# Performance work log

Measured on AMD Instinct MI355X. Metric: run time of the kernel, lower is better.

The kernel has to match this reference:

```python
import jax, jax.numpy as jnp
import numpy as np

N = 8192  # number of candidates being ranked


def setup_inputs() -> dict:
    key = jax.random.key(0)
    k1, k2 = jax.random.split(key)
    logits = jax.random.normal(k1, (N,), dtype=jnp.float32)
    rankings = jax.random.randint(k2, (N,), 0, N).astype(jnp.int64)
    return {"logits": logits, "rankings": rankings}


def reference(logits, rankings):
    # Vectorized WeightedRankNetLoss:
    #   loss = (1/N) * sum_{i<j, r_i<r_j} log(1 + exp(logits[j]-logits[i])) / (r_i + r_j)
    n = logits.shape[0]
    idx = jnp.arange(n)
    # pair selected iff i < j AND rankings[i] < rankings[j]
    pair_mask = (idx[:, None] < idx[None, :]) & (rankings[:, None] < rankings[None, :])
    r = rankings.astype(logits.dtype)
    rsum = r[:, None] + r[None, :]
    # For selected pairs r_j >= r_i + 1 >= 1, so rsum >= 1; clamp only protects masked entries.
    w = jnp.where(pair_mask, 1.0, 0.0) / jnp.maximum(rsum, 1.0)  # [N, N]
    d = logits[None, :] - logits[:, None]  # d[i, j] = logits[j] - logits[i]
    loss = jnp.sum(w * jax.nn.softplus(d))  # softplus = log(1+exp(.)), numerically stable
    return loss / n
```

## Files before the change

### kernel.cpp

```cpp
#include <hip/hip_runtime.h>

#define N_CAND 8192
#define TILE   128
#define NTILES (N_CAND / TILE)
#define NLIVE  (NTILES * (NTILES + 1) / 2)

__global__ __launch_bounds__(TILE) void ranknet_pairs_kernel(
    const float* __restrict__ logits,
    const int*   __restrict__ rankings,
    float*       __restrict__ partials)
{
    const int t = blockIdx.x;
    int bj = (int)((__builtin_sqrtf(8.0f * (float)t + 1.0f) - 1.0f) * 0.5f);
    while ((bj + 1) * (bj + 2) / 2 <= t) ++bj;
    while (bj * (bj + 1) / 2 > t)       --bj;
    const int bi = t - bj * (bj + 1) / 2;

    __shared__ float2 s_j[TILE];
    __shared__ float  s_part[TILE / 64];

    const float LOG2E = 1.4426950408889634f;
    const int tid = threadIdx.x;

    const int i = bi * TILE + tid;
    const float lis = logits[i] * LOG2E;
    const float ri  = (float)rankings[i];

    const int j = bj * TILE + tid;
    s_j[tid] = make_float2(logits[j] * LOG2E, (float)rankings[j]);
    __syncthreads();

    float acc = 0.0f;
    if (bi != bj) {
        #pragma unroll 8
        for (int jj = 0; jj < TILE; ++jj) {
            const float2 v = s_j[jj];
            const float dl = v.x - lis;
            const float e  = __builtin_exp2f(-fabsf(dl));
            const float sp = fmaxf(dl, 0.0f) + __builtin_log2f(1.0f + e);
            const float w  = (v.y > ri) ? __builtin_amdgcn_rcpf(ri + v.y) : 0.0f;
            acc = fmaf(w, sp, acc);
        }
    } else {
        #pragma unroll 8
        for (int jj = 0; jj < TILE; ++jj) {
            const float2 v = s_j[jj];
            const float dl = v.x - lis;
            const float e  = __builtin_exp2f(-fabsf(dl));
            const float sp = fmaxf(dl, 0.0f) + __builtin_log2f(1.0f + e);
            const bool act = (jj > tid) && (v.y > ri);
            const float w  = act ? __builtin_amdgcn_rcpf(ri + v.y) : 0.0f;
            acc = fmaf(w, sp, acc);
        }
    }

    #pragma unroll
    for (int off = 32; off > 0; off >>= 1)
        acc += __shfl_down(acc, off, 64);
    if ((tid & 63) == 0) s_part[tid >> 6] = acc;
    __syncthreads();
    if (tid == 0) {
        float s = 0.0f;
        #pragma unroll
        for (int w = 0; w < TILE / 64; ++w) s += s_part[w];
        partials[t] = s;
    }
}

__global__ __launch_bounds__(256) void ranknet_reduce_kernel(
    const float* __restrict__ partials,
    float*       __restrict__ out)
{
    __shared__ float s_part[4];
    const int tid = threadIdx.x;

    float acc = 0.0f;
    for (int k = tid; k < NLIVE; k += 256)
        acc += partials[k];

    #pragma unroll
    for (int off = 32; off > 0; off >>= 1)
        acc += __shfl_down(acc, off, 64);
    if ((tid & 63) == 0) s_part[tid >> 6] = acc;
    __syncthreads();
    if (tid == 0) {
        float s = s_part[0] + s_part[1] + s_part[2] + s_part[3];
        const float LN2 = 0.6931471805599453f;
        out[0] = s * (LN2 / (float)N_CAND);
    }
}

extern "C" void kernel_launch(void* const* d_in, const int* in_sizes, int n_in,
                              void* d_out, int out_size, void* d_ws, size_t ws_size,
                              hipStream_t stream)
{
    const float* logits   = (const float*)d_in[0];
    const int*   rankings = (const int*)  d_in[1];
    float*       out      = (float*)d_out;
    float*       partials = (float*)d_ws;

    ranknet_pairs_kernel<<<dim3(NLIVE), dim3(TILE), 0, stream>>>(logits, rankings, partials);
    ranknet_reduce_kernel<<<1, 256, 0, stream>>>(partials, out);
}
```

Before: 84.21 us.

## Use single-wave tiles with readlane broadcast and a cheaper softplus formulation

```diff
diff --git a/kernel.cpp b/kernel.cpp
--- a/kernel.cpp
+++ b/kernel.cpp
@@ -1,9 +1,13 @@
 #include <hip/hip_runtime.h>
 
 #define N_CAND 8192
-#define TILE   128
+#define TILE   64
 #define NTILES (N_CAND / TILE)
 #define NLIVE  (NTILES * (NTILES + 1) / 2)
+
+__device__ __forceinline__ float readlane_f(float x, int lane) {
+    return __int_as_float(__builtin_amdgcn_readlane(__float_as_int(x), lane));
+}
 
 __global__ __launch_bounds__(TILE) void ranknet_pairs_kernel(
     const float* __restrict__ logits,
@@ -16,43 +20,78 @@
     while (bj * (bj + 1) / 2 > t)       --bj;
     const int bi = t - bj * (bj + 1) / 2;
 
-    __shared__ float2 s_j[TILE];
-    __shared__ float  s_part[TILE / 64];
+    const float LOG2E = 1.4426950408889634f;
+    const float INF   = __builtin_inff();
+    const int lane = threadIdx.x;
 
-    const float LOG2E = 1.4426950408889634f;
+    const float lis = logits[bi * TILE + lane] * LOG2E;
+    const float ri  = (float)rankings[bi * TILE + lane];
+    const float ljv = logits[bj * TILE + lane] * LOG2E;
+    const float rjv = (float)rankings[bj * TILE + lane];
+
+    float acc0 = 0.0f, acc1 = 0.0f;
+    if (bi != bj) {
+        #pragma unroll
+        for (int jj = 0; jj < TILE; jj += 2) {
+            {
+                const float lj = readlane_f(ljv, jj);
+                const float rj = readlane_f(rjv, jj);
+                const float dl = lj - lis;
+                const float sp = __builtin_amdgcn_logf(1.0f + __builtin_amdgcn_exp2f(dl));
+                const float rs = (rj > ri) ? (ri + rj) : INF;
+                acc0 = fmaf(__builtin_amdgcn_rcpf(rs), sp, acc0);
+            }
+            {
+                const float lj = readlane_f(ljv, jj + 1);
+                const float rj = readlane_f(rjv, jj + 1);
+                const float dl = lj - lis;
+                const float sp = __builtin_amdgcn_logf(1.0f + __builtin_amdgcn_exp2f(dl));
+                const float rs = (rj > ri) ? (ri + rj) : INF;
+                acc1 = fmaf(__builtin_amdgcn_rcpf(rs), sp, acc1);
+            }
+        }
+    } else {
+        #pragma unroll
+        for (int jj = 0; jj < TILE; jj += 2) {
+            {
+                const float lj = readlane_f(ljv, jj);
+                const float rj = readlane_f(rjv, jj);
+                const float dl = lj - lis;
+                const float sp = __builtin_amdgcn_logf(1.0f + __builtin_amdgcn_exp2f(dl));
+                const bool act = (jj > lane) && (rj > ri);
+                const float rs = act ? (ri + rj) : INF;
+                acc0 = fmaf(__builtin_amdgcn_rcpf(rs), sp, acc0);
+            }
+            {
+                const float lj = readlane_f(ljv, jj + 1);
+                const float rj = readlane_f(rjv, jj + 1);
+                const float dl = lj - lis;
+                const float sp = __builtin_amdgcn_logf(1.0f + __builtin_amdgcn_exp2f(dl));
+                const bool act = (jj + 1 > lane) && (rj > ri);
+                const float rs = act ? (ri + rj) : INF;
+                acc1 = fmaf(__builtin_amdgcn_rcpf(rs), sp, acc1);
+            }
+        }
+    }
+
+    float acc = acc0 + acc1;
+    #pragma unroll
+    for (int off = 32; off > 0; off >>= 1)
+        acc += __shfl_down(acc, off, 64);
+    if (lane == 0)
+        partials[t] = acc;
+}
+
+__global__ __launch_bounds__(1024) void ranknet_reduce_kernel(
+    const float* __restrict__ partials,
+    float*       __restrict__ out)
+{
+    __shared__ float s_part[16];
     const int tid = threadIdx.x;
 
-    const int i = bi * TILE + tid;
-    const float lis = logits[i] * LOG2E;
-    const float ri  = (float)rankings[i];
-
-    const int j = bj * TILE + tid;
-    s_j[tid] = make_float2(logits[j] * LOG2E, (float)rankings[j]);
-    __syncthreads();
-
     float acc = 0.0f;
-    if (bi != bj) {
-        #pragma unroll 8
-        for (int jj = 0; jj < TILE; ++jj) {
-            const float2 v = s_j[jj];
-            const float dl = v.x - lis;
-            const float e  = __builtin_exp2f(-fabsf(dl));
-            const float sp = fmaxf(dl, 0.0f) + __builtin_log2f(1.0f + e);
-            const float w  = (v.y > ri) ? __builtin_amdgcn_rcpf(ri + v.y) : 0.0f;
-            acc = fmaf(w, sp, acc);
-        }
-    } else {
-        #pragma unroll 8
-        for (int jj = 0; jj < TILE; ++jj) {
-            const float2 v = s_j[jj];
-            const float dl = v.x - lis;
-            const float e  = __builtin_exp2f(-fabsf(dl));
-            const float sp = fmaxf(dl, 0.0f) + __builtin_log2f(1.0f + e);
-            const bool act = (jj > tid) && (v.y > ri);
-            const float w  = act ? __builtin_amdgcn_rcpf(ri + v.y) : 0.0f;
-            acc = fmaf(w, sp, acc);
-        }
-    }
+    for (int k = tid; k < NLIVE; k += 1024)
+        acc += partials[k];
 
     #pragma unroll
     for (int off = 32; off > 0; off >>= 1)
@@ -62,29 +101,7 @@
     if (tid == 0) {
         float s = 0.0f;
         #pragma unroll
-        for (int w = 0; w < TILE / 64; ++w) s += s_part[w];
-        partials[t] = s;
-    }
-}
-
-__global__ __launch_bounds__(256) void ranknet_reduce_kernel(
-    const float* __restrict__ partials,
-    float*       __restrict__ out)
-{
-    __shared__ float s_part[4];
-    const int tid = threadIdx.x;
-
-    float acc = 0.0f;
-    for (int k = tid; k < NLIVE; k += 256)
-        acc += partials[k];
-
-    #pragma unroll
-    for (int off = 32; off > 0; off >>= 1)
-        acc += __shfl_down(acc, off, 64);
-    if ((tid & 63) == 0) s_part[tid >> 6] = acc;
-    __syncthreads();
-    if (tid == 0) {
-        float s = s_part[0] + s_part[1] + s_part[2] + s_part[3];
+        for (int w = 0; w < 16; ++w) s += s_part[w];
         const float LN2 = 0.6931471805599453f;
         out[0] = s * (LN2 / (float)N_CAND);
     }
@@ -100,5 +117,5 @@
     float*       partials = (float*)d_ws;
 
     ranknet_pairs_kernel<<<dim3(NLIVE), dim3(TILE), 0, stream>>>(logits, rankings, partials);
-    ranknet_reduce_kernel<<<1, 256, 0, stream>>>(partials, out);
+    ranknet_reduce_kernel<<<1, 1024, 0, stream>>>(partials, out);
 }
```

Result: faster. 72.56 us (-13.8%).
